# Performance work log

Hardware: AMD Instinct MI355X
Metric: run time of the kernel (lower is better)

## Reference

```python
import jax, jax.numpy as jnp
import numpy as np

B, NA, D, H = 64, 32, 128, 6  # scenes, agents/scene, out_dim, heads
N = B * NA
E = B * NA * NA


def layer_norm(x, g, b, eps=1e-5):
    m = jnp.mean(x, axis=-1, keepdims=True)
    v = jnp.var(x, axis=-1, keepdims=True)
    return (x - m) * jax.lax.rsqrt(v + eps) * g + b


def setup_inputs() -> dict:
    key = jax.random.key(0)
    ks = jax.random.split(key, 10)
    # fully-connected edges within each scene
    ids = jnp.arange(N, dtype=jnp.int32).reshape(B, NA)
    hi = jnp.broadcast_to(ids[:, :, None], (B, NA, NA)).reshape(-1)  # repeat 'd -> (d n)'
    wi = jnp.broadcast_to(ids[:, None, :], (B, NA, NA)).reshape(-1)  # repeat 'd -> (n d)'
    s_in = 1.0 / np.sqrt(D)
    s_hd = 1.0 / np.sqrt(H * D)
    return {
        'agents': jax.random.normal(ks[0], (N, D), jnp.float32),
        'hi': hi, 'wi': wi,
        'Wq': jax.random.normal(ks[1], (H * D, D), jnp.float32) * s_in,
        'gq': jnp.ones((H * D,), jnp.float32), 'bq': jnp.zeros((H * D,), jnp.float32),
        'Wk': jax.random.normal(ks[2], (H * D, D), jnp.float32) * s_in,
        'gk': jnp.ones((H * D,), jnp.float32), 'bk': jnp.zeros((H * D,), jnp.float32),
        'Wv': jax.random.normal(ks[3], (H * D, D), jnp.float32) * s_in,
        'gv': jnp.ones((H * D,), jnp.float32), 'bv': jnp.zeros((H * D,), jnp.float32),
        'Wo1': jax.random.normal(ks[4], (D, H * D), jnp.float32) * s_hd,
        'go': jnp.ones((D,), jnp.float32), 'bo': jnp.zeros((D,), jnp.float32),
        'Wo2': jax.random.normal(ks[5], (D, D), jnp.float32) * s_in,
        'W1': jax.random.normal(ks[6], (D, D), jnp.float32) * s_in,
        'gn': jnp.ones((D,), jnp.float32), 'bn': jnp.zeros((D,), jnp.float32),
        'W2': jax.random.normal(ks[7], (D, D), jnp.float32) * s_in,
    }


def reference(agents, hi, wi, Wq, gq, bq, Wk, gk, bk, Wv, gv, bv, Wo1, go, bo, Wo2, W1, gn, bn, W2):
    n, d = agents.shape
    scale = d ** -0.5
    xh = agents[hi]                                   # [E, D]
    xw = agents[wi]                                   # [E, D]
    q = layer_norm(xh @ Wq.T, gq, bq).reshape(-1, H, d)                 # [E, H, D]
    k = layer_norm(xw @ Wk.T, gk, bk).reshape(-1, H, d)
    v = jax.nn.relu(layer_norm(xw @ Wv.T, gv, bv)).reshape(-1, H, d)
    att = jnp.sum(q * k, axis=-1) * scale             # [E, H] per-edge score
    att = jnp.exp(att - jnp.max(att))                 # global max, as in original
    att_sum = jax.ops.segment_sum(att, hi, num_segments=n)   # [N, H]
    att = att / att_sum[hi]
    out = jax.ops.segment_sum(att[..., None] * v, hi, num_segments=n)   # [N, H, D]
    out = out.reshape(n, H * d)
    out = jax.nn.relu(layer_norm(out @ Wo1.T, go, bo)) @ Wo2.T          # to_out
    nodes = agents @ W1.T
    nodes = jax.nn.relu(layer_norm(nodes + out, gn, bn))
    nodes = nodes @ W2.T
    return jax.nn.relu(nodes + agents)
```

## Files before the change

### kernel.cpp

```cpp
#include <hip/hip_runtime.h>
#include <math.h>

#define NN 2048
#define HH 6
#define HD 768
#define NA 32
#define NB 64
#define KC 3

typedef __bf16 bf16x8 __attribute__((ext_vector_type(8)));
typedef float  f32x4  __attribute__((ext_vector_type(4)));

__device__ __forceinline__ float dot4(float4 a, float4 b) {
    return a.x * b.x + a.y * b.y + a.z * b.z + a.w * b.w;
}

__device__ __forceinline__ void split2(float f, ushort& h, ushort& l) {
    const uint u = __float_as_uint(f);
    h = (ushort)(u >> 16);
    const float hf = __uint_as_float((uint)h << 16);
    l = (ushort)(__float_as_uint(f - hf) >> 16);
}

__global__ __launch_bounds__(256) void split_kernel(
    const float* __restrict__ agents, const float* __restrict__ Wq,
    const float* __restrict__ Wk, const float* __restrict__ Wv,
    const float* __restrict__ Wo1,
    ushort* __restrict__ Ahi, ushort* __restrict__ Alo,
    ushort* __restrict__ Whi, ushort* __restrict__ Wlo,
    ushort* __restrict__ W1hi, ushort* __restrict__ W1lo)
{
    const int y = blockIdx.y;
    const float* src;
    ushort *dh, *dl;
    int n4;
    if (y == 0)      { src = agents; dh = Ahi;  dl = Alo;  n4 = NN * 128 / 4; }
    else if (y == 4) { src = Wo1;    dh = W1hi; dl = W1lo; n4 = 128 * HD / 4; }
    else {
        src = (y == 1) ? Wq : (y == 2) ? Wk : Wv;
        dh = Whi + (size_t)(y - 1) * 768 * 128;
        dl = Wlo + (size_t)(y - 1) * 768 * 128;
        n4 = 768 * 128 / 4;
    }
    const int i = blockIdx.x * 256 + threadIdx.x;
    if (i < n4) {
        const float4 v = ((const float4*)src)[i];
        ushort4 h, l;
        split2(v.x, h.x, l.x);
        split2(v.y, h.y, l.y);
        split2(v.z, h.z, l.z);
        split2(v.w, h.w, l.w);
        ((ushort4*)dh)[i] = h;
        ((ushort4*)dl)[i] = l;
    }
}

__global__ __launch_bounds__(256) void proj_mfma_kernel(
    const ushort* __restrict__ Ahi, const ushort* __restrict__ Alo,
    const ushort* __restrict__ Whi, const ushort* __restrict__ Wlo,
    float* __restrict__ R)
{
    const int tid = threadIdx.x;
    const int wave = tid >> 6, lane = tid & 63;
    const int row0 = blockIdx.x * 64 + wave * 16;
    const int cb0  = blockIdx.y * 64;
    const int lrow = lane & 15, kq = lane >> 4;
    const int koff = kq * 8;

    const ushort* ah = Ahi + (size_t)(row0 + lrow) * 128 + koff;
    const ushort* al = Alo + (size_t)(row0 + lrow) * 128 + koff;

    f32x4 acc[4];
    #pragma unroll
    for (int ct = 0; ct < 4; ++ct)
        #pragma unroll
        for (int j = 0; j < 4; ++j) acc[ct][j] = 0.f;

    #pragma unroll
    for (int kt = 0; kt < 4; ++kt) {
        const bf16x8 avh = *(const bf16x8*)(ah + kt * 32);
        const bf16x8 avl = *(const bf16x8*)(al + kt * 32);
        #pragma unroll
        for (int ct = 0; ct < 4; ++ct) {
            const size_t wof = (size_t)(cb0 + ct * 16 + lrow) * 128 + koff + kt * 32;
            const bf16x8 bvh = *(const bf16x8*)(Whi + wof);
            const bf16x8 bvl = *(const bf16x8*)(Wlo + wof);
            acc[ct] = __builtin_amdgcn_mfma_f32_16x16x32_bf16(avh, bvh, acc[ct], 0, 0, 0);
            acc[ct] = __builtin_amdgcn_mfma_f32_16x16x32_bf16(avh, bvl, acc[ct], 0, 0, 0);
            acc[ct] = __builtin_amdgcn_mfma_f32_16x16x32_bf16(avl, bvh, acc[ct], 0, 0, 0);
        }
    }

    #pragma unroll
    for (int ct = 0; ct < 4; ++ct) {
        const int colg = cb0 + ct * 16;
        const int m = colg / 768;
        const int c = colg - m * 768 + lrow;
        float* rp = R + ((size_t)m * NN + row0 + kq * 4) * HD + c;
        #pragma unroll
        for (int j = 0; j < 4; ++j)
            rp[(size_t)j * HD] = acc[ct][j];
    }
}

__global__ __launch_bounds__(256) void stats_kernel(
    const float* __restrict__ R, float* __restrict__ ps)
{
    const int wave = threadIdx.x >> 6, lane = threadIdx.x & 63;
    const int rr = blockIdx.x * 4 + wave;
    const float4* rp = (const float4*)(R + (size_t)rr * HD);
    float s = 0.f, q = 0.f;
    #pragma unroll
    for (int r = 0; r < 3; ++r) {
        const float4 v = rp[lane + r * 64];
        s += v.x + v.y + v.z + v.w;
        q += v.x * v.x + v.y * v.y + v.z * v.z + v.w * v.w;
    }
    #pragma unroll
    for (int mask = 32; mask >= 1; mask >>= 1) {
        s += __shfl_xor(s, mask);
        q += __shfl_xor(q, mask);
    }
    if (lane == 0) { ps[(size_t)rr * 2] = s; ps[(size_t)rr * 2 + 1] = q; }
}

__global__ __launch_bounds__(256) void attn_kernel(
    const float* __restrict__ R, const float* __restrict__ ps,
    const float* __restrict__ gq, const float* __restrict__ bq,
    const float* __restrict__ gk, const float* __restrict__ bk,
    const float* __restrict__ gv, const float* __restrict__ bv,
    ushort* __restrict__ Ohi, ushort* __restrict__ Olo)
{
    __shared__ float Qs[32][132];
    __shared__ float Ks[32][132];
    __shared__ float Vs[32][132];
    __shared__ float Ss[32][33];
    __shared__ float stat_s[3][32][2];
    const int tid = threadIdx.x;
    const int scene = blockIdx.x, h = blockIdx.y;

    if (tid < 96) {
        const int m = tid / 32, row = tid & 31;
        const float* p = ps + ((size_t)m * NN + scene * 32 + row) * 2;
        const float mu  = p[0] * (1.f / 768.f);
        const float var = p[1] * (1.f / 768.f) - mu * mu;
        stat_s[m][row][0] = mu;
        stat_s[m][row][1] = rsqrtf(var + 1e-5f);
    }
    __syncthreads();

    for (int m = 0; m < 3; ++m) {
        const float* Rm = R + (size_t)m * NN * HD;
        const float* g = (m == 0) ? gq : (m == 1) ? gk : gv;
        const float* b = (m == 0) ? bq : (m == 1) ? bk : bv;
        float* dst = (m == 0) ? &Qs[0][0] : (m == 1) ? &Ks[0][0] : &Vs[0][0];
        #pragma unroll
        for (int r = 0; r < 4; ++r) {
            const int idx = tid + r * 256;
            const int row = idx >> 5, c4 = idx & 31;
            const float4 x = *(const float4*)(Rm + ((size_t)scene * 32 + row) * HD + h * 128 + c4 * 4);
            const float mu = stat_s[m][row][0], rs = stat_s[m][row][1];
            const float4 gg = *(const float4*)(g + h * 128 + c4 * 4);
            const float4 bb = *(const float4*)(b + h * 128 + c4 * 4);
            float4 y;
            y.x = (x.x - mu) * rs * gg.x + bb.x;
            y.y = (x.y - mu) * rs * gg.y + bb.y;
            y.z = (x.z - mu) * rs * gg.z + bb.z;
            y.w = (x.w - mu) * rs * gg.w + bb.w;
            if (m == 2) {
                y.x = fmaxf(y.x, 0.f); y.y = fmaxf(y.y, 0.f);
                y.z = fmaxf(y.z, 0.f); y.w = fmaxf(y.w, 0.f);
            }
            *(float4*)(dst + row * 132 + c4 * 4) = y;
        }
    }
    __syncthreads();

    {
        const int ti = tid >> 4, tj = tid & 15;
        float a00 = 0.f, a01 = 0.f, a10 = 0.f, a11 = 0.f;
        #pragma unroll 4
        for (int k4 = 0; k4 < 32; ++k4) {
            const float4 q0 = *(const float4*)&Qs[2 * ti][k4 * 4];
            const float4 q1 = *(const float4*)&Qs[2 * ti + 1][k4 * 4];
            const float4 k0 = *(const float4*)&Ks[2 * tj][k4 * 4];
            const float4 k1 = *(const float4*)&Ks[2 * tj + 1][k4 * 4];
            a00 += dot4(q0, k0); a01 += dot4(q0, k1);
            a10 += dot4(q1, k0); a11 += dot4(q1, k1);
        }
        const float scale = 0.08838834764831845f;
        Ss[2 * ti][2 * tj]         = a00 * scale;
        Ss[2 * ti][2 * tj + 1]     = a01 * scale;
        Ss[2 * ti + 1][2 * tj]     = a10 * scale;
        Ss[2 * ti + 1][2 * tj + 1] = a11 * scale;
    }
    __syncthreads();

    {
        const int g = tid >> 5, l = tid & 31;
        #pragma unroll
        for (int ib = 0; ib < 4; ++ib) {
            const int i = g + ib * 8;
            const float sv = Ss[i][l];
            float mx = sv;
            #pragma unroll
            for (int mask = 16; mask >= 1; mask >>= 1)
                mx = fmaxf(mx, __shfl_xor(mx, mask));
            const float p = __expf(sv - mx);
            float sum = p;
            #pragma unroll
            for (int mask = 16; mask >= 1; mask >>= 1)
                sum += __shfl_xor(sum, mask);
            Ss[i][l] = p / sum;
        }
    }
    __syncthreads();

    {
        const int i = tid >> 3, dg = tid & 7;
        float o[4][4] = {};
        for (int j = 0; j < 32; ++j) {
            const float p = Ss[i][j];
            #pragma unroll
            for (int r = 0; r < 4; ++r) {
                const float4 v4 = *(const float4*)&Vs[j][dg * 4 + 32 * r];
                o[r][0] += p * v4.x; o[r][1] += p * v4.y;
                o[r][2] += p * v4.z; o[r][3] += p * v4.w;
            }
        }
        const size_t base = ((size_t)scene * 32 + i) * HD + h * 128;
        #pragma unroll
        for (int r = 0; r < 4; ++r) {
            ushort4 hs, ls;
            split2(o[r][0], hs.x, ls.x);
            split2(o[r][1], hs.y, ls.y);
            split2(o[r][2], hs.z, ls.z);
            split2(o[r][3], hs.w, ls.w);
            *(ushort4*)(Ohi + base + dg * 4 + 32 * r) = hs;
            *(ushort4*)(Olo + base + dg * 4 + 32 * r) = ls;
        }
    }
}

__global__ __launch_bounds__(256) void wo1_mfma_kernel(
    const ushort* __restrict__ Ohi, const ushort* __restrict__ Olo,
    const ushort* __restrict__ W1hi, const ushort* __restrict__ W1lo,
    float* __restrict__ P)
{
    const int tid = threadIdx.x;
    const int wave = tid >> 6, lane = tid & 63;
    const int row0 = blockIdx.x * 64 + wave * 16;
    const int col0 = blockIdx.y * 16;
    const int kb   = blockIdx.z * 256;
    const int lrow = lane & 15, kq = lane >> 4;
    const int koff = kq * 8;

    const ushort* ah = Ohi  + (size_t)(row0 + lrow) * HD + kb + koff;
    const ushort* al = Olo  + (size_t)(row0 + lrow) * HD + kb + koff;
    const ushort* bh = W1hi + (size_t)(col0 + lrow) * HD + kb + koff;
    const ushort* bl = W1lo + (size_t)(col0 + lrow) * HD + kb + koff;

    f32x4 acc;
    #pragma unroll
    for (int j = 0; j < 4; ++j) acc[j] = 0.f;

    #pragma unroll
    for (int kt = 0; kt < 8; ++kt) {
        const bf16x8 avh = *(const bf16x8*)(ah + kt * 32);
        const bf16x8 avl = *(const bf16x8*)(al + kt * 32);
        const bf16x8 bvh = *(const bf16x8*)(bh + kt * 32);
        const bf16x8 bvl = *(const bf16x8*)(bl + kt * 32);
        acc = __builtin_amdgcn_mfma_f32_16x16x32_bf16(avh, bvh, acc, 0, 0, 0);
        acc = __builtin_amdgcn_mfma_f32_16x16x32_bf16(avh, bvl, acc, 0, 0, 0);
        acc = __builtin_amdgcn_mfma_f32_16x16x32_bf16(avl, bvh, acc, 0, 0, 0);
    }

    float* pp = P + ((size_t)blockIdx.z * NN + row0 + kq * 4) * 128 + col0 + lrow;
    #pragma unroll
    for (int j = 0; j < 4; ++j)
        pp[(size_t)j * 128] = acc[j];
}

__global__ __launch_bounds__(128) void epilogue_kernel(
    const float* __restrict__ P, const float* __restrict__ agents,
    const float* __restrict__ go, const float* __restrict__ bo,
    const float* __restrict__ Wo2, const float* __restrict__ W1,
    const float* __restrict__ gn, const float* __restrict__ bn,
    const float* __restrict__ W2, float* __restrict__ out)
{
    __shared__ float As[8][132];
    __shared__ float ts[8][132];
    __shared__ float zs[8][132];
    __shared__ float red[2][8][2];
    const int tid = threadIdx.x;
    const int cg = tid >> 3, n = tid & 7;
    const int n0 = blockIdx.x * 8;
    const int colbase = cg * 8;

    {
        const float4* src = (const float4*)(agents + (size_t)n0 * 128);
        #pragma unroll
        for (int r = 0; r < 2; ++r) {
            const int idx = tid + r * 128;
            const int row = idx >> 5, c4 = idx & 31;
            *(float4*)&As[row][c4 * 4] = src[idx];
        }
    }

    float acc[8] = {0.f, 0.f, 0.f, 0.f, 0.f, 0.f, 0.f, 0.f};
    {
        #pragma unroll
        for (int kcc = 0; kcc < KC; ++kcc) {
            const float* p = P + ((size_t)kcc * NN + n0 + n) * 128 + colbase;
            const float4 a = *(const float4*)p;
            const float4 b = *(const float4*)(p + 4);
            acc[0] += a.x; acc[1] += a.y; acc[2] += a.z; acc[3] += a.w;
            acc[4] += b.x; acc[5] += b.y; acc[6] += b.z; acc[7] += b.w;
        }
    }

    {
        float s = 0.f, q = 0.f;
        #pragma unroll
        for (int jj = 0; jj < 8; ++jj) { s += acc[jj]; q += acc[jj] * acc[jj]; }
        #pragma unroll
        for (int mask = 8; mask <= 32; mask <<= 1) {
            s += __shfl_xor(s, mask); q += __shfl_xor(q, mask);
        }
        if ((tid & 63) < 8) { red[tid >> 6][tid & 7][0] = s; red[tid >> 6][tid & 7][1] = q; }
        __syncthreads();
        const float st = red[0][n][0] + red[1][n][0];
        const float qt = red[0][n][1] + red[1][n][1];
        const float mu = st * (1.f / 128.f);
        const float var = qt * (1.f / 128.f) - mu * mu;
        const float rs = rsqrtf(var + 1e-5f);
        float t[8];
        #pragma unroll
        for (int jj = 0; jj < 8; ++jj) {
            const int c = colbase + jj;
            t[jj] = fmaxf((acc[jj] - mu) * rs * go[c] + bo[c], 0.f);
        }
        *(float4*)&ts[n][colbase]     = make_float4(t[0], t[1], t[2], t[3]);
        *(float4*)&ts[n][colbase + 4] = make_float4(t[4], t[5], t[6], t[7]);
    }
    __syncthreads();

    float acc2[8] = {0.f, 0.f, 0.f, 0.f, 0.f, 0.f, 0.f, 0.f};
    for (int k4 = 0; k4 < 32; ++k4) {
        const float4 t4 = *(const float4*)&ts[n][k4 * 4];
        const float4 a4 = *(const float4*)&As[n][k4 * 4];
        #pragma unroll
        for (int jj = 0; jj < 8; ++jj) {
            const float4 w2 = *(const float4*)(Wo2 + (size_t)(colbase + jj) * 128 + k4 * 4);
            const float4 w1 = *(const float4*)(W1 + (size_t)(colbase + jj) * 128 + k4 * 4);
            acc2[jj] += dot4(t4, w2) + dot4(a4, w1);
        }
    }

    {
        float s = 0.f, q = 0.f;
        #pragma unroll
        for (int jj = 0; jj < 8; ++jj) { s += acc2[jj]; q += acc2[jj] * acc2[jj]; }
        #pragma unroll
        for (int mask = 8; mask <= 32; mask <<= 1) {
            s += __shfl_xor(s, mask); q += __shfl_xor(q, mask);
        }
        __syncthreads();
        if ((tid & 63) < 8) { red[tid >> 6][tid & 7][0] = s; red[tid >> 6][tid & 7][1] = q; }
        __syncthreads();
        const float st = red[0][n][0] + red[1][n][0];
        const float qt = red[0][n][1] + red[1][n][1];
        const float mu = st * (1.f / 128.f);
        const float var = qt * (1.f / 128.f) - mu * mu;
        const float rs = rsqrtf(var + 1e-5f);
        float z[8];
        #pragma unroll
        for (int jj = 0; jj < 8; ++jj) {
            const int c = colbase + jj;
            z[jj] = fmaxf((acc2[jj] - mu) * rs * gn[c] + bn[c], 0.f);
        }
        *(float4*)&zs[n][colbase]     = make_float4(z[0], z[1], z[2], z[3]);
        *(float4*)&zs[n][colbase + 4] = make_float4(z[4], z[5], z[6], z[7]);
    }
    __syncthreads();

    float acc3[8] = {0.f, 0.f, 0.f, 0.f, 0.f, 0.f, 0.f, 0.f};
    for (int k4 = 0; k4 < 32; ++k4) {
        const float4 z4 = *(const float4*)&zs[n][k4 * 4];
        #pragma unroll
        for (int jj = 0; jj < 8; ++jj) {
            const float4 w = *(const float4*)(W2 + (size_t)(colbase + jj) * 128 + k4 * 4);
            acc3[jj] += dot4(z4, w);
        }
    }
    const float4 ar0 = *(const float4*)&As[n][colbase];
    const float4 ar1 = *(const float4*)&As[n][colbase + 4];
    float* op = out + ((size_t)n0 + n) * 128 + colbase;
    *(float4*)op = make_float4(fmaxf(acc3[0] + ar0.x, 0.f), fmaxf(acc3[1] + ar0.y, 0.f),
                               fmaxf(acc3[2] + ar0.z, 0.f), fmaxf(acc3[3] + ar0.w, 0.f));
    *(float4*)(op + 4) = make_float4(fmaxf(acc3[4] + ar1.x, 0.f), fmaxf(acc3[5] + ar1.y, 0.f),
                                     fmaxf(acc3[6] + ar1.z, 0.f), fmaxf(acc3[7] + ar1.w, 0.f));
}

extern "C" void kernel_launch(void* const* d_in, const int* in_sizes, int n_in,
                              void* d_out, int out_size, void* d_ws, size_t ws_size,
                              hipStream_t stream) {
    (void)in_sizes; (void)n_in; (void)out_size; (void)ws_size;
    const float* agents = (const float*)d_in[0];
    const float* Wq  = (const float*)d_in[3];
    const float* gq  = (const float*)d_in[4];
    const float* bq  = (const float*)d_in[5];
    const float* Wk  = (const float*)d_in[6];
    const float* gk  = (const float*)d_in[7];
    const float* bk  = (const float*)d_in[8];
    const float* Wv  = (const float*)d_in[9];
    const float* gv  = (const float*)d_in[10];
    const float* bv  = (const float*)d_in[11];
    const float* Wo1 = (const float*)d_in[12];
    const float* go  = (const float*)d_in[13];
    const float* bo  = (const float*)d_in[14];
    const float* Wo2 = (const float*)d_in[15];
    const float* W1  = (const float*)d_in[16];
    const float* gn  = (const float*)d_in[17];
    const float* bn  = (const float*)d_in[18];
    const float* W2  = (const float*)d_in[19];
    float* out = (float*)d_out;

    float* ws = (float*)d_ws;
    float* R  = ws;
    float* P  = R;
    float* ps = R + (size_t)3 * NN * HD;
    ushort* u = (ushort*)(ps + (size_t)2 * 3 * NN);
    ushort* Ohi  = u;  u += (size_t)NN * HD;
    ushort* Olo  = u;  u += (size_t)NN * HD;
    ushort* Ahi  = u;  u += (size_t)NN * 128;
    ushort* Alo  = u;  u += (size_t)NN * 128;
    ushort* Whi  = u;  u += (size_t)3 * 768 * 128;
    ushort* Wlo  = u;  u += (size_t)3 * 768 * 128;
    ushort* W1hi = u;  u += (size_t)128 * HD;
    ushort* W1lo = u;  u += (size_t)128 * HD;

    split_kernel<<<dim3(256, 5), 256, 0, stream>>>(agents, Wq, Wk, Wv, Wo1,
                                                   Ahi, Alo, Whi, Wlo, W1hi, W1lo);
    proj_mfma_kernel<<<dim3(32, 36), 256, 0, stream>>>(Ahi, Alo, Whi, Wlo, R);
    stats_kernel<<<1536, 256, 0, stream>>>(R, ps);
    attn_kernel<<<dim3(NB, HH), 256, 0, stream>>>(R, ps, gq, bq, gk, bk, gv, bv, Ohi, Olo);
    wo1_mfma_kernel<<<dim3(32, 8, 3), 256, 0, stream>>>(Ohi, Olo, W1hi, W1lo, P);
    epilogue_kernel<<<NN / 8, 128, 0, stream>>>(P, agents, go, bo, Wo2, W1, gn, bn, W2, out);
}
```

Baseline: 173.5 us.

## Move attention and epilogue matmuls onto split-bf16 MFMA

The per-scene attention kernel is rewritten as single-wave blocks that apply layernorm inline, split Q/K/V into hi/lo bf16 pairs, and compute the scores and the P·V product with 16x16x32 bf16 MFMA (three-term split), using shared memory only for the softmax probabilities. The epilogue's three 128x128 matmuls (Wo2, W1, W2) likewise move from scalar FP32 dot products to split-bf16 MFMA, and the split kernel now also pre-splits Wo2, W1 and W2. The aim is to replace FP32 ALU work with matrix-core throughput. In exchange there are fewer threads per block, V is loaded from global memory with strided scalar reads, and the three-term split carries some precision risk.

```diff
diff --git a/kernel.cpp b/kernel.cpp
--- a/kernel.cpp
+++ b/kernel.cpp
@@ -6,14 +6,9 @@
 #define HD 768
 #define NA 32
 #define NB 64
-#define KC 3
 
 typedef __bf16 bf16x8 __attribute__((ext_vector_type(8)));
 typedef float  f32x4  __attribute__((ext_vector_type(4)));
-
-__device__ __forceinline__ float dot4(float4 a, float4 b) {
-    return a.x * b.x + a.y * b.y + a.z * b.z + a.w * b.w;
-}
 
 __device__ __forceinline__ void split2(float f, ushort& h, ushort& l) {
     const uint u = __float_as_uint(f);
@@ -22,25 +17,64 @@
     l = (ushort)(__float_as_uint(f - hf) >> 16);
 }
 
+__device__ __forceinline__ bf16x8 pack8(const ushort* s) {
+    uint4 u;
+    u.x = (uint)s[0] | ((uint)s[1] << 16);
+    u.y = (uint)s[2] | ((uint)s[3] << 16);
+    u.z = (uint)s[4] | ((uint)s[5] << 16);
+    u.w = (uint)s[6] | ((uint)s[7] << 16);
+    return *(bf16x8*)&u;
+}
+
+__device__ __forceinline__ void ln8_split(
+    const float* __restrict__ x, float mu, float rs,
+    const float* __restrict__ g, const float* __restrict__ b,
+    bf16x8& hi, bf16x8& lo)
+{
+    const float4 x0 = *(const float4*)x;
+    const float4 x1 = *(const float4*)(x + 4);
+    const float4 g0 = *(const float4*)g;
+    const float4 g1 = *(const float4*)(g + 4);
+    const float4 b0 = *(const float4*)b;
+    const float4 b1 = *(const float4*)(b + 4);
+    ushort hh[8], ll[8];
+    float v;
+    v = (x0.x - mu) * rs * g0.x + b0.x; split2(v, hh[0], ll[0]);
+    v = (x0.y - mu) * rs * g0.y + b0.y; split2(v, hh[1], ll[1]);
+    v = (x0.z - mu) * rs * g0.z + b0.z; split2(v, hh[2], ll[2]);
+    v = (x0.w - mu) * rs * g0.w + b0.w; split2(v, hh[3], ll[3]);
+    v = (x1.x - mu) * rs * g1.x + b1.x; split2(v, hh[4], ll[4]);
+    v = (x1.y - mu) * rs * g1.y + b1.y; split2(v, hh[5], ll[5]);
+    v = (x1.z - mu) * rs * g1.z + b1.z; split2(v, hh[6], ll[6]);
+    v = (x1.w - mu) * rs * g1.w + b1.w; split2(v, hh[7], ll[7]);
+    hi = pack8(hh); lo = pack8(ll);
+}
+
 __global__ __launch_bounds__(256) void split_kernel(
     const float* __restrict__ agents, const float* __restrict__ Wq,
     const float* __restrict__ Wk, const float* __restrict__ Wv,
-    const float* __restrict__ Wo1,
+    const float* __restrict__ Wo1, const float* __restrict__ Wo2,
+    const float* __restrict__ W1, const float* __restrict__ W2,
     ushort* __restrict__ Ahi, ushort* __restrict__ Alo,
     ushort* __restrict__ Whi, ushort* __restrict__ Wlo,
-    ushort* __restrict__ W1hi, ushort* __restrict__ W1lo)
+    ushort* __restrict__ Wo1hi, ushort* __restrict__ Wo1lo,
+    ushort* __restrict__ Wo2hi, ushort* __restrict__ Wo2lo,
+    ushort* __restrict__ W1hi, ushort* __restrict__ W1lo,
+    ushort* __restrict__ W2hi, ushort* __restrict__ W2lo)
 {
     const int y = blockIdx.y;
     const float* src;
     ushort *dh, *dl;
     int n4;
-    if (y == 0)      { src = agents; dh = Ahi;  dl = Alo;  n4 = NN * 128 / 4; }
-    else if (y == 4) { src = Wo1;    dh = W1hi; dl = W1lo; n4 = 128 * HD / 4; }
-    else {
-        src = (y == 1) ? Wq : (y == 2) ? Wk : Wv;
-        dh = Whi + (size_t)(y - 1) * 768 * 128;
-        dl = Wlo + (size_t)(y - 1) * 768 * 128;
-        n4 = 768 * 128 / 4;
+    switch (y) {
+        case 0:  src = agents; dh = Ahi;   dl = Alo;   n4 = NN * 128 / 4;  break;
+        case 1:  src = Wq;  dh = Whi;                dl = Wlo;                n4 = 768*128/4; break;
+        case 2:  src = Wk;  dh = Whi + 768*128;      dl = Wlo + 768*128;      n4 = 768*128/4; break;
+        case 3:  src = Wv;  dh = Whi + 2*768*128;    dl = Wlo + 2*768*128;    n4 = 768*128/4; break;
+        case 4:  src = Wo1; dh = Wo1hi; dl = Wo1lo;  n4 = 128 * HD / 4;  break;
+        case 5:  src = Wo2; dh = Wo2hi; dl = Wo2lo;  n4 = 128 * 128 / 4; break;
+        case 6:  src = W1;  dh = W1hi;  dl = W1lo;   n4 = 128 * 128 / 4; break;
+        default: src = W2;  dh = W2hi;  dl = W2lo;   n4 = 128 * 128 / 4; break;
     }
     const int i = blockIdx.x * 256 + threadIdx.x;
     if (i < n4) {
@@ -124,127 +158,131 @@
     if (lane == 0) { ps[(size_t)rr * 2] = s; ps[(size_t)rr * 2 + 1] = q; }
 }
 
-__global__ __launch_bounds__(256) void attn_kernel(
+__global__ __launch_bounds__(64) void attn_mfma_kernel(
     const float* __restrict__ R, const float* __restrict__ ps,
     const float* __restrict__ gq, const float* __restrict__ bq,
     const float* __restrict__ gk, const float* __restrict__ bk,
     const float* __restrict__ gv, const float* __restrict__ bv,
     ushort* __restrict__ Ohi, ushort* __restrict__ Olo)
 {
-    __shared__ float Qs[32][132];
-    __shared__ float Ks[32][132];
-    __shared__ float Vs[32][132];
-    __shared__ float Ss[32][33];
-    __shared__ float stat_s[3][32][2];
-    const int tid = threadIdx.x;
-    const int scene = blockIdx.x, h = blockIdx.y;
-
-    if (tid < 96) {
-        const int m = tid / 32, row = tid & 31;
-        const float* p = ps + ((size_t)m * NN + scene * 32 + row) * 2;
-        const float mu  = p[0] * (1.f / 768.f);
-        const float var = p[1] * (1.f / 768.f) - mu * mu;
-        stat_s[m][row][0] = mu;
-        stat_s[m][row][1] = rsqrtf(var + 1e-5f);
+    __shared__ ushort phi[16][40];
+    __shared__ ushort plo[16][40];
+    const int lane = threadIdx.x;
+    const int lrow = lane & 15, kq = lane >> 4;
+    const int scene = blockIdx.x, h = blockIdx.y, rt = blockIdx.z;
+    const int brow = scene * 32;
+
+    const float* Rq = R;
+    const float* Rk = R + (size_t)NN * HD;
+    const float* Rv = R + (size_t)2 * NN * HD;
+
+    const int qrow = brow + rt * 16 + lrow;
+    const float2 sq_ = *(const float2*)(ps + (size_t)qrow * 2);
+    const float muq = sq_.x * (1.f / 768.f);
+    const float rsq = rsqrtf(sq_.y * (1.f / 768.f) - muq * muq + 1e-5f);
+
+    float muk[2], rsk[2];
+    #pragma unroll
+    for (int ct = 0; ct < 2; ++ct) {
+        const int krow = brow + ct * 16 + lrow;
+        const float2 sk_ = *(const float2*)(ps + (size_t)(NN + krow) * 2);
+        muk[ct] = sk_.x * (1.f / 768.f);
+        rsk[ct] = rsqrtf(sk_.y * (1.f / 768.f) - muk[ct] * muk[ct] + 1e-5f);
+    }
+    float muv[8], rsv[8];
+    #pragma unroll
+    for (int j = 0; j < 8; ++j) {
+        const int vrow = brow + kq * 8 + j;
+        const float2 sv_ = *(const float2*)(ps + (size_t)(2 * NN + vrow) * 2);
+        muv[j] = sv_.x * (1.f / 768.f);
+        rsv[j] = rsqrtf(sv_.y * (1.f / 768.f) - muv[j] * muv[j] + 1e-5f);
+    }
+
+    f32x4 s[2];
+    #pragma unroll
+    for (int ct = 0; ct < 2; ++ct)
+        #pragma unroll
+        for (int j = 0; j < 4; ++j) s[ct][j] = 0.f;
+
+    #pragma unroll
+    for (int kt = 0; kt < 4; ++kt) {
+        const int c0 = h * 128 + kt * 32 + kq * 8;
+        bf16x8 qh, ql;
+        ln8_split(Rq + (size_t)qrow * HD + c0, muq, rsq, gq + c0, bq + c0, qh, ql);
+        #pragma unroll
+        for (int ct = 0; ct < 2; ++ct) {
+            bf16x8 kh, kl;
+            ln8_split(Rk + (size_t)(brow + ct * 16 + lrow) * HD + c0, muk[ct], rsk[ct],
+                      gk + c0, bk + c0, kh, kl);
+            s[ct] = __builtin_amdgcn_mfma_f32_16x16x32_bf16(qh, kh, s[ct], 0, 0, 0);
+            s[ct] = __builtin_amdgcn_mfma_f32_16x16x32_bf16(qh, kl, s[ct], 0, 0, 0);
+            s[ct] = __builtin_amdgcn_mfma_f32_16x16x32_bf16(ql, kh, s[ct], 0, 0, 0);
+        }
+    }
+
+    const float scl = 0.08838834764831845f;
+    float p0[4], p1[4];
+    #pragma unroll
+    for (int j = 0; j < 4; ++j) {
+        const float a = s[0][j] * scl, b = s[1][j] * scl;
+        float m = fmaxf(a, b);
+        #pragma unroll
+        for (int msk = 1; msk <= 8; msk <<= 1) m = fmaxf(m, __shfl_xor(m, msk));
+        const float ea = __expf(a - m), eb = __expf(b - m);
+        float su = ea + eb;
+        #pragma unroll
+        for (int msk = 1; msk <= 8; msk <<= 1) su += __shfl_xor(su, msk);
+        const float inv = 1.f / su;
+        p0[j] = ea * inv;
+        p1[j] = eb * inv;
+    }
+
+    #pragma unroll
+    for (int j = 0; j < 4; ++j) {
+        ushort hh, ll;
+        split2(p0[j], hh, ll);
+        phi[kq * 4 + j][lrow] = hh;
+        plo[kq * 4 + j][lrow] = ll;
+        split2(p1[j], hh, ll);
+        phi[kq * 4 + j][16 + lrow] = hh;
+        plo[kq * 4 + j][16 + lrow] = ll;
     }
     __syncthreads();
-
-    for (int m = 0; m < 3; ++m) {
-        const float* Rm = R + (size_t)m * NN * HD;
-        const float* g = (m == 0) ? gq : (m == 1) ? gk : gv;
-        const float* b = (m == 0) ? bq : (m == 1) ? bk : bv;
-        float* dst = (m == 0) ? &Qs[0][0] : (m == 1) ? &Ks[0][0] : &Vs[0][0];
-        #pragma unroll
-        for (int r = 0; r < 4; ++r) {
-            const int idx = tid + r * 256;
-            const int row = idx >> 5, c4 = idx & 31;
-            const float4 x = *(const float4*)(Rm + ((size_t)scene * 32 + row) * HD + h * 128 + c4 * 4);
-            const float mu = stat_s[m][row][0], rs = stat_s[m][row][1];
-            const float4 gg = *(const float4*)(g + h * 128 + c4 * 4);
-            const float4 bb = *(const float4*)(b + h * 128 + c4 * 4);
-            float4 y;
-            y.x = (x.x - mu) * rs * gg.x + bb.x;
-            y.y = (x.y - mu) * rs * gg.y + bb.y;
-            y.z = (x.z - mu) * rs * gg.z + bb.z;
-            y.w = (x.w - mu) * rs * gg.w + bb.w;
-            if (m == 2) {
-                y.x = fmaxf(y.x, 0.f); y.y = fmaxf(y.y, 0.f);
-                y.z = fmaxf(y.z, 0.f); y.w = fmaxf(y.w, 0.f);
-            }
-            *(float4*)(dst + row * 132 + c4 * 4) = y;
-        }
-    }
-    __syncthreads();
-
-    {
-        const int ti = tid >> 4, tj = tid & 15;
-        float a00 = 0.f, a01 = 0.f, a10 = 0.f, a11 = 0.f;
-        #pragma unroll 4
-        for (int k4 = 0; k4 < 32; ++k4) {
-            const float4 q0 = *(const float4*)&Qs[2 * ti][k4 * 4];
-            const float4 q1 = *(const float4*)&Qs[2 * ti + 1][k4 * 4];
-            const float4 k0 = *(const float4*)&Ks[2 * tj][k4 * 4];
-            const float4 k1 = *(const float4*)&Ks[2 * tj + 1][k4 * 4];
-            a00 += dot4(q0, k0); a01 += dot4(q0, k1);
-            a10 += dot4(q1, k0); a11 += dot4(q1, k1);
-        }
-        const float scale = 0.08838834764831845f;
-        Ss[2 * ti][2 * tj]         = a00 * scale;
-        Ss[2 * ti][2 * tj + 1]     = a01 * scale;
-        Ss[2 * ti + 1][2 * tj]     = a10 * scale;
-        Ss[2 * ti + 1][2 * tj + 1] = a11 * scale;
-    }
-    __syncthreads();
-
-    {
-        const int g = tid >> 5, l = tid & 31;
-        #pragma unroll
-        for (int ib = 0; ib < 4; ++ib) {
-            const int i = g + ib * 8;
-            const float sv = Ss[i][l];
-            float mx = sv;
-            #pragma unroll
-            for (int mask = 16; mask >= 1; mask >>= 1)
-                mx = fmaxf(mx, __shfl_xor(mx, mask));
-            const float p = __expf(sv - mx);
-            float sum = p;
-            #pragma unroll
-            for (int mask = 16; mask >= 1; mask >>= 1)
-                sum += __shfl_xor(sum, mask);
-            Ss[i][l] = p / sum;
-        }
-    }
-    __syncthreads();
-
-    {
-        const int i = tid >> 3, dg = tid & 7;
-        float o[4][4] = {};
-        for (int j = 0; j < 32; ++j) {
-            const float p = Ss[i][j];
-            #pragma unroll
-            for (int r = 0; r < 4; ++r) {
-                const float4 v4 = *(const float4*)&Vs[j][dg * 4 + 32 * r];
-                o[r][0] += p * v4.x; o[r][1] += p * v4.y;
-                o[r][2] += p * v4.z; o[r][3] += p * v4.w;
-            }
-        }
-        const size_t base = ((size_t)scene * 32 + i) * HD + h * 128;
-        #pragma unroll
-        for (int r = 0; r < 4; ++r) {
-            ushort4 hs, ls;
-            split2(o[r][0], hs.x, ls.x);
-            split2(o[r][1], hs.y, ls.y);
-            split2(o[r][2], hs.z, ls.z);
-            split2(o[r][3], hs.w, ls.w);
-            *(ushort4*)(Ohi + base + dg * 4 + 32 * r) = hs;
-            *(ushort4*)(Olo + base + dg * 4 + 32 * r) = ls;
+    const bf16x8 pah = *(const bf16x8*)&phi[lrow][kq * 8];
+    const bf16x8 pal = *(const bf16x8*)&plo[lrow][kq * 8];
+
+    #pragma unroll
+    for (int dt = 0; dt < 8; ++dt) {
+        const int d = h * 128 + dt * 16 + lrow;
+        const float gvd = gv[d], bvd = bv[d];
+        ushort vh[8], vl[8];
+        #pragma unroll
+        for (int j = 0; j < 8; ++j) {
+            const float x = Rv[(size_t)(brow + kq * 8 + j) * HD + d];
+            const float v = fmaxf((x - muv[j]) * rsv[j] * gvd + bvd, 0.f);
+            split2(v, vh[j], vl[j]);
+        }
+        const bf16x8 bh = pack8(vh), bl = pack8(vl);
+        f32x4 o;
+        #pragma unroll
+        for (int j = 0; j < 4; ++j) o[j] = 0.f;
+        o = __builtin_amdgcn_mfma_f32_16x16x32_bf16(pah, bh, o, 0, 0, 0);
+        o = __builtin_amdgcn_mfma_f32_16x16x32_bf16(pah, bl, o, 0, 0, 0);
+        o = __builtin_amdgcn_mfma_f32_16x16x32_bf16(pal, bh, o, 0, 0, 0);
+        #pragma unroll
+        for (int j = 0; j < 4; ++j) {
+            const size_t oo = (size_t)(brow + rt * 16 + kq * 4 + j) * HD + d;
+            ushort hh, ll;
+            split2(o[j], hh, ll);
+            Ohi[oo] = hh;
+            Olo[oo] = ll;
         }
     }
 }
 
 __global__ __launch_bounds__(256) void wo1_mfma_kernel(
     const ushort* __restrict__ Ohi, const ushort* __restrict__ Olo,
-    const ushort* __restrict__ W1hi, const ushort* __restrict__ W1lo,
+    const ushort* __restrict__ Wo1hi, const ushort* __restrict__ Wo1lo,
     float* __restrict__ P)
 {
     const int tid = threadIdx.x;
@@ -255,10 +293,10 @@
     const int lrow = lane & 15, kq = lane >> 4;
     const int koff = kq * 8;
 
-    const ushort* ah = Ohi  + (size_t)(row0 + lrow) * HD + kb + koff;
-    const ushort* al = Olo  + (size_t)(row0 + lrow) * HD + kb + koff;
-    const ushort* bh = W1hi + (size_t)(col0 + lrow) * HD + kb + koff;
-    const ushort* bl = W1lo + (size_t)(col0 + lrow) * HD + kb + koff;
+    const ushort* ah = Ohi   + (size_t)(row0 + lrow) * HD + kb + koff;
+    const ushort* al = Olo   + (size_t)(row0 + lrow) * HD + kb + koff;
+    const ushort* bh = Wo1hi + (size_t)(col0 + lrow) * HD + kb + koff;
+    const ushort* bl = Wo1lo + (size_t)(col0 + lrow) * HD + kb + koff;
 
     f32x4 acc;
     #pragma unroll
@@ -281,125 +319,153 @@
         pp[(size_t)j * 128] = acc[j];
 }
 
-__global__ __launch_bounds__(128) void epilogue_kernel(
-    const float* __restrict__ P, const float* __restrict__ agents,
+__global__ __launch_bounds__(64) void epilogue_mfma_kernel(
+    const float* __restrict__ P,
+    const ushort* __restrict__ Ahi, const ushort* __restrict__ Alo,
+    const float* __restrict__ agents,
     const float* __restrict__ go, const float* __restrict__ bo,
-    const float* __restrict__ Wo2, const float* __restrict__ W1,
+    const ushort* __restrict__ Wo2hi, const ushort* __restrict__ Wo2lo,
+    const ushort* __restrict__ W1hi, const ushort* __restrict__ W1lo,
     const float* __restrict__ gn, const float* __restrict__ bn,
-    const float* __restrict__ W2, float* __restrict__ out)
-{
-    __shared__ float As[8][132];
-    __shared__ float ts[8][132];
-    __shared__ float zs[8][132];
-    __shared__ float red[2][8][2];
-    const int tid = threadIdx.x;
-    const int cg = tid >> 3, n = tid & 7;
-    const int n0 = blockIdx.x * 8;
-    const int colbase = cg * 8;
-
-    {
-        const float4* src = (const float4*)(agents + (size_t)n0 * 128);
-        #pragma unroll
-        for (int r = 0; r < 2; ++r) {
-            const int idx = tid + r * 128;
-            const int row = idx >> 5, c4 = idx & 31;
-            *(float4*)&As[row][c4 * 4] = src[idx];
-        }
-    }
-
-    float acc[8] = {0.f, 0.f, 0.f, 0.f, 0.f, 0.f, 0.f, 0.f};
-    {
-        #pragma unroll
-        for (int kcc = 0; kcc < KC; ++kcc) {
-            const float* p = P + ((size_t)kcc * NN + n0 + n) * 128 + colbase;
-            const float4 a = *(const float4*)p;
-            const float4 b = *(const float4*)(p + 4);
-            acc[0] += a.x; acc[1] += a.y; acc[2] += a.z; acc[3] += a.w;
-            acc[4] += b.x; acc[5] += b.y; acc[6] += b.z; acc[7] += b.w;
-        }
-    }
-
-    {
-        float s = 0.f, q = 0.f;
-        #pragma unroll
-        for (int jj = 0; jj < 8; ++jj) { s += acc[jj]; q += acc[jj] * acc[jj]; }
-        #pragma unroll
-        for (int mask = 8; mask <= 32; mask <<= 1) {
-            s += __shfl_xor(s, mask); q += __shfl_xor(q, mask);
-        }
-        if ((tid & 63) < 8) { red[tid >> 6][tid & 7][0] = s; red[tid >> 6][tid & 7][1] = q; }
-        __syncthreads();
-        const float st = red[0][n][0] + red[1][n][0];
-        const float qt = red[0][n][1] + red[1][n][1];
-        const float mu = st * (1.f / 128.f);
-        const float var = qt * (1.f / 128.f) - mu * mu;
-        const float rs = rsqrtf(var + 1e-5f);
-        float t[8];
-        #pragma unroll
-        for (int jj = 0; jj < 8; ++jj) {
-            const int c = colbase + jj;
-            t[jj] = fmaxf((acc[jj] - mu) * rs * go[c] + bo[c], 0.f);
-        }
-        *(float4*)&ts[n][colbase]     = make_float4(t[0], t[1], t[2], t[3]);
-        *(float4*)&ts[n][colbase + 4] = make_float4(t[4], t[5], t[6], t[7]);
+    const ushort* __restrict__ W2hi, const ushort* __restrict__ W2lo,
+    float* __restrict__ out)
+{
+    __shared__ float zb[16][132];
+    const int lane = threadIdx.x;
+    const int lrow = lane & 15, kq = lane >> 4;
+    const int n0 = blockIdx.x * 16;
+    const int nodeA = n0 + lrow;
+
+    float tv[4][8];
+    float s = 0.f, q = 0.f;
+    #pragma unroll
+    for (int kt = 0; kt < 4; ++kt) {
+        const int c0 = kt * 32 + kq * 8;
+        const float* pp0 = P + (size_t)nodeA * 128 + c0;
+        const float* pp1 = pp0 + (size_t)NN * 128;
+        const float* pp2 = pp1 + (size_t)NN * 128;
+        #pragma unroll
+        for (int hf = 0; hf < 2; ++hf) {
+            const float4 a = *(const float4*)(pp0 + hf * 4);
+            const float4 b = *(const float4*)(pp1 + hf * 4);
+            const float4 c = *(const float4*)(pp2 + hf * 4);
+            tv[kt][hf * 4 + 0] = a.x + b.x + c.x;
+            tv[kt][hf * 4 + 1] = a.y + b.y + c.y;
+            tv[kt][hf * 4 + 2] = a.z + b.z + c.z;
+            tv[kt][hf * 4 + 3] = a.w + b.w + c.w;
+        }
+        #pragma unroll
+        for (int j = 0; j < 8; ++j) { s += tv[kt][j]; q += tv[kt][j] * tv[kt][j]; }
+    }
+    s += __shfl_xor(s, 16); s += __shfl_xor(s, 32);
+    q += __shfl_xor(q, 16); q += __shfl_xor(q, 32);
+    const float mu = s * (1.f / 128.f);
+    const float rs = rsqrtf(q * (1.f / 128.f) - mu * mu + 1e-5f);
+
+    bf16x8 th[4], tl[4], ah[4], al[4];
+    #pragma unroll
+    for (int kt = 0; kt < 4; ++kt) {
+        const int c0 = kt * 32 + kq * 8;
+        const float4 g0 = *(const float4*)(go + c0);
+        const float4 g1 = *(const float4*)(go + c0 + 4);
+        const float4 b0 = *(const float4*)(bo + c0);
+        const float4 b1 = *(const float4*)(bo + c0 + 4);
+        const float gg[8] = {g0.x, g0.y, g0.z, g0.w, g1.x, g1.y, g1.z, g1.w};
+        const float bb[8] = {b0.x, b0.y, b0.z, b0.w, b1.x, b1.y, b1.z, b1.w};
+        ushort hh[8], ll[8];
+        #pragma unroll
+        for (int j = 0; j < 8; ++j) {
+            const float v = fmaxf((tv[kt][j] - mu) * rs * gg[j] + bb[j], 0.f);
+            split2(v, hh[j], ll[j]);
+        }
+        th[kt] = pack8(hh); tl[kt] = pack8(ll);
+        ah[kt] = *(const bf16x8*)(Ahi + (size_t)nodeA * 128 + c0);
+        al[kt] = *(const bf16x8*)(Alo + (size_t)nodeA * 128 + c0);
+    }
+
+    f32x4 u[8];
+    #pragma unroll
+    for (int ct = 0; ct < 8; ++ct)
+        #pragma unroll
+        for (int j = 0; j < 4; ++j) u[ct][j] = 0.f;
+
+    #pragma unroll
+    for (int ct = 0; ct < 8; ++ct) {
+        const size_t wb = (size_t)(ct * 16 + lrow) * 128;
+        #pragma unroll
+        for (int kt = 0; kt < 4; ++kt) {
+            const int c0 = kt * 32 + kq * 8;
+            const bf16x8 wh = *(const bf16x8*)(Wo2hi + wb + c0);
+            const bf16x8 wl = *(const bf16x8*)(Wo2lo + wb + c0);
+            const bf16x8 vh = *(const bf16x8*)(W1hi + wb + c0);
+            const bf16x8 vl = *(const bf16x8*)(W1lo + wb + c0);
+            u[ct] = __builtin_amdgcn_mfma_f32_16x16x32_bf16(th[kt], wh, u[ct], 0, 0, 0);
+            u[ct] = __builtin_amdgcn_mfma_f32_16x16x32_bf16(th[kt], wl, u[ct], 0, 0, 0);
+            u[ct] = __builtin_amdgcn_mfma_f32_16x16x32_bf16(tl[kt], wh, u[ct], 0, 0, 0);
+            u[ct] = __builtin_amdgcn_mfma_f32_16x16x32_bf16(ah[kt], vh, u[ct], 0, 0, 0);
+            u[ct] = __builtin_amdgcn_mfma_f32_16x16x32_bf16(ah[kt], vl, u[ct], 0, 0, 0);
+            u[ct] = __builtin_amdgcn_mfma_f32_16x16x32_bf16(al[kt], vh, u[ct], 0, 0, 0);
+        }
+    }
+
+    float gnc[8], bnc[8];
+    #pragma unroll
+    for (int ct = 0; ct < 8; ++ct) {
+        gnc[ct] = gn[ct * 16 + lrow];
+        bnc[ct] = bn[ct * 16 + lrow];
+    }
+    #pragma unroll
+    for (int j = 0; j < 4; ++j) {
+        float s2 = 0.f, q2 = 0.f;
+        #pragma unroll
+        for (int ct = 0; ct < 8; ++ct) { const float v = u[ct][j]; s2 += v; q2 += v * v; }
+        #pragma unroll
+        for (int msk = 1; msk <= 8; msk <<= 1) {
+            s2 += __shfl_xor(s2, msk);
+            q2 += __shfl_xor(q2, msk);
+        }
+        const float mu2 = s2 * (1.f / 128.f);
+        const float rs2 = rsqrtf(q2 * (1.f / 128.f) - mu2 * mu2 + 1e-5f);
+        #pragma unroll
+        for (int ct = 0; ct < 8; ++ct)
+            zb[kq * 4 + j][ct * 16 + lrow] =
+                fmaxf((u[ct][j] - mu2) * rs2 * gnc[ct] + bnc[ct], 0.f);
     }
     __syncthreads();
 
-    float acc2[8] = {0.f, 0.f, 0.f, 0.f, 0.f, 0.f, 0.f, 0.f};
-    for (int k4 = 0; k4 < 32; ++k4) {
-        const float4 t4 = *(const float4*)&ts[n][k4 * 4];
-        const float4 a4 = *(const float4*)&As[n][k4 * 4];
-        #pragma unroll
-        for (int jj = 0; jj < 8; ++jj) {
-            const float4 w2 = *(const float4*)(Wo2 + (size_t)(colbase + jj) * 128 + k4 * 4);
-            const float4 w1 = *(const float4*)(W1 + (size_t)(colbase + jj) * 128 + k4 * 4);
-            acc2[jj] += dot4(t4, w2) + dot4(a4, w1);
-        }
-    }
-
-    {
-        float s = 0.f, q = 0.f;
-        #pragma unroll
-        for (int jj = 0; jj < 8; ++jj) { s += acc2[jj]; q += acc2[jj] * acc2[jj]; }
-        #pragma unroll
-        for (int mask = 8; mask <= 32; mask <<= 1) {
-            s += __shfl_xor(s, mask); q += __shfl_xor(q, mask);
-        }
-        __syncthreads();
-        if ((tid & 63) < 8) { red[tid >> 6][tid & 7][0] = s; red[tid >> 6][tid & 7][1] = q; }
-        __syncthreads();
-        const float st = red[0][n][0] + red[1][n][0];
-        const float qt = red[0][n][1] + red[1][n][1];
-        const float mu = st * (1.f / 128.f);
-        const float var = qt * (1.f / 128.f) - mu * mu;
-        const float rs = rsqrtf(var + 1e-5f);
-        float z[8];
-        #pragma unroll
-        for (int jj = 0; jj < 8; ++jj) {
-            const int c = colbase + jj;
-            z[jj] = fmaxf((acc2[jj] - mu) * rs * gn[c] + bn[c], 0.f);
-        }
-        *(float4*)&zs[n][colbase]     = make_float4(z[0], z[1], z[2], z[3]);
-        *(float4*)&zs[n][colbase + 4] = make_float4(z[4], z[5], z[6], z[7]);
-    }
-    __syncthreads();
-
-    float acc3[8] = {0.f, 0.f, 0.f, 0.f, 0.f, 0.f, 0.f, 0.f};
-    for (int k4 = 0; k4 < 32; ++k4) {
-        const float4 z4 = *(const float4*)&zs[n][k4 * 4];
-        #pragma unroll
-        for (int jj = 0; jj < 8; ++jj) {
-            const float4 w = *(const float4*)(W2 + (size_t)(colbase + jj) * 128 + k4 * 4);
-            acc3[jj] += dot4(z4, w);
-        }
-    }
-    const float4 ar0 = *(const float4*)&As[n][colbase];
-    const float4 ar1 = *(const float4*)&As[n][colbase + 4];
-    float* op = out + ((size_t)n0 + n) * 128 + colbase;
-    *(float4*)op = make_float4(fmaxf(acc3[0] + ar0.x, 0.f), fmaxf(acc3[1] + ar0.y, 0.f),
-                               fmaxf(acc3[2] + ar0.z, 0.f), fmaxf(acc3[3] + ar0.w, 0.f));
-    *(float4*)(op + 4) = make_float4(fmaxf(acc3[4] + ar1.x, 0.f), fmaxf(acc3[5] + ar1.y, 0.f),
-                                     fmaxf(acc3[6] + ar1.z, 0.f), fmaxf(acc3[7] + ar1.w, 0.f));
+    bf16x8 zh[4], zl[4];
+    #pragma unroll
+    for (int kt = 0; kt < 4; ++kt) {
+        const int c0 = kt * 32 + kq * 8;
+        const float4 z0 = *(const float4*)&zb[lrow][c0];
+        const float4 z1 = *(const float4*)&zb[lrow][c0 + 4];
+        const float zz[8] = {z0.x, z0.y, z0.z, z0.w, z1.x, z1.y, z1.z, z1.w};
+        ushort hh[8], ll[8];
+        #pragma unroll
+        for (int j = 0; j < 8; ++j) split2(zz[j], hh[j], ll[j]);
+        zh[kt] = pack8(hh); zl[kt] = pack8(ll);
+    }
+    #pragma unroll
+    for (int ct = 0; ct < 8; ++ct) {
+        f32x4 o;
+        #pragma unroll
+        for (int j = 0; j < 4; ++j) o[j] = 0.f;
+        const size_t wb = (size_t)(ct * 16 + lrow) * 128;
+        #pragma unroll
+        for (int kt = 0; kt < 4; ++kt) {
+            const int c0 = kt * 32 + kq * 8;
+            const bf16x8 wh = *(const bf16x8*)(W2hi + wb + c0);
+            const bf16x8 wl = *(const bf16x8*)(W2lo + wb + c0);
+            o = __builtin_amdgcn_mfma_f32_16x16x32_bf16(zh[kt], wh, o, 0, 0, 0);
+            o = __builtin_amdgcn_mfma_f32_16x16x32_bf16(zh[kt], wl, o, 0, 0, 0);
+            o = __builtin_amdgcn_mfma_f32_16x16x32_bf16(zl[kt], wh, o, 0, 0, 0);
+        }
+        #pragma unroll
+        for (int j = 0; j < 4; ++j) {
+            const size_t oo = (size_t)(n0 + kq * 4 + j) * 128 + ct * 16 + lrow;
+            out[oo] = fmaxf(o[j] + agents[oo], 0.f);
+        }
+    }
 }
 
 extern "C" void kernel_launch(void* const* d_in, const int* in_sizes, int n_in,
@@ -428,23 +494,32 @@
 
     float* ws = (float*)d_ws;
     float* R  = ws;
-    float* P  = R;
+    float* Pp = R;
     float* ps = R + (size_t)3 * NN * HD;
     ushort* u = (ushort*)(ps + (size_t)2 * 3 * NN);
-    ushort* Ohi  = u;  u += (size_t)NN * HD;
-    ushort* Olo  = u;  u += (size_t)NN * HD;
-    ushort* Ahi  = u;  u += (size_t)NN * 128;
-    ushort* Alo  = u;  u += (size_t)NN * 128;
-    ushort* Whi  = u;  u += (size_t)3 * 768 * 128;
-    ushort* Wlo  = u;  u += (size_t)3 * 768 * 128;
-    ushort* W1hi = u;  u += (size_t)128 * HD;
-    ushort* W1lo = u;  u += (size_t)128 * HD;
-
-    split_kernel<<<dim3(256, 5), 256, 0, stream>>>(agents, Wq, Wk, Wv, Wo1,
-                                                   Ahi, Alo, Whi, Wlo, W1hi, W1lo);
+    ushort* Ohi   = u;  u += (size_t)NN * HD;
+    ushort* Olo   = u;  u += (size_t)NN * HD;
+    ushort* Ahi   = u;  u += (size_t)NN * 128;
+    ushort* Alo   = u;  u += (size_t)NN * 128;
+    ushort* Whi   = u;  u += (size_t)3 * 768 * 128;
+    ushort* Wlo   = u;  u += (size_t)3 * 768 * 128;
+    ushort* Wo1hi = u;  u += (size_t)128 * HD;
+    ushort* Wo1lo = u;  u += (size_t)128 * HD;
+    ushort* Wo2hi = u;  u += (size_t)128 * 128;
+    ushort* Wo2lo = u;  u += (size_t)128 * 128;
+    ushort* W1hi  = u;  u += (size_t)128 * 128;
+    ushort* W1lo  = u;  u += (size_t)128 * 128;
+    ushort* W2hi  = u;  u += (size_t)128 * 128;
+    ushort* W2lo  = u;  u += (size_t)128 * 128;
+
+    split_kernel<<<dim3(256, 8), 256, 0, stream>>>(
+        agents, Wq, Wk, Wv, Wo1, Wo2, W1, W2,
+        Ahi, Alo, Whi, Wlo, Wo1hi, Wo1lo, Wo2hi, Wo2lo, W1hi, W1lo, W2hi, W2lo);
     proj_mfma_kernel<<<dim3(32, 36), 256, 0, stream>>>(Ahi, Alo, Whi, Wlo, R);
     stats_kernel<<<1536, 256, 0, stream>>>(R, ps);
-    attn_kernel<<<dim3(NB, HH), 256, 0, stream>>>(R, ps, gq, bq, gk, bk, gv, bv, Ohi, Olo);
-    wo1_mfma_kernel<<<dim3(32, 8, 3), 256, 0, stream>>>(Ohi, Olo, W1hi, W1lo, P);
-    epilogue_kernel<<<NN / 8, 128, 0, stream>>>(P, agents, go, bo, Wo2, W1, gn, bn, W2, out);
-}
+    attn_mfma_kernel<<<dim3(64, 6, 2), 64, 0, stream>>>(R, ps, gq, bq, gk, bk, gv, bv, Ohi, Olo);
+    wo1_mfma_kernel<<<dim3(32, 8, 3), 256, 0, stream>>>(Ohi, Olo, Wo1hi, Wo1lo, Pp);
+    epilogue_mfma_kernel<<<128, 64, 0, stream>>>(Pp, Ahi, Alo, agents, go, bo,
+                                                 Wo2hi, Wo2lo, W1hi, W1lo, gn, bn,
+                                                 W2hi, W2lo, out);
+}
```

Result: no change. 170.8 us (-1.5%).
